# Performance work log

Measured on AMD Instinct MI355X. Metric: run time of the kernel, lower is better.

Reference implementation:

```python
import jax, jax.numpy as jnp
import numpy as np

TOPK = 10
NUM_CLASSES = 80
ALPHA = 0.5
BETA = 6.0
EPS = 1e-9


def setup_inputs() -> dict:
    key = jax.random.key(0)
    ks = jax.random.split(key, 7)
    bs, A, n, C = 16, 8400, 64, NUM_CLASSES
    pd_scores = jax.random.uniform(ks[0], (bs, A, C), jnp.float32)
    # valid xyxy boxes inside a 640x640 image
    pxy = jax.random.uniform(ks[1], (bs, A, 2), jnp.float32) * 576.0
    pwh = jax.random.uniform(ks[2], (bs, A, 2), jnp.float32) * 64.0 + 8.0
    pd_bboxes = jnp.concatenate([pxy, pxy + pwh], axis=-1)
    gxy = jax.random.uniform(ks[3], (bs, n, 2), jnp.float32) * 576.0
    gwh = jax.random.uniform(ks[4], (bs, n, 2), jnp.float32) * 64.0 + 8.0
    gt_bboxes = jnp.concatenate([gxy, gxy + gwh], axis=-1)
    anc_points = jax.random.uniform(ks[5], (A, 2), jnp.float32) * 640.0
    gt_labels = jax.random.randint(ks[6], (bs, n, 1), 0, C, dtype=jnp.int32)
    return {"pd_scores": pd_scores, "pd_bboxes": pd_bboxes,
            "anc_points": anc_points, "gt_labels": gt_labels,
            "gt_bboxes": gt_bboxes}


def _iou(gt_bboxes, pd_bboxes, eps=EPS):
    # gt_bboxes: (bs, n, 4), pd_bboxes: (bs, A, 4) -> (bs, n, A)
    b1 = gt_bboxes[:, :, None, :]
    b2 = pd_bboxes[:, None, :, :]
    lt = jnp.maximum(b1[..., :2], b2[..., :2])
    rb = jnp.minimum(b1[..., 2:], b2[..., 2:])
    overlap = jnp.clip(rb - lt, 0).prod(-1)
    area1 = jnp.clip(b1[..., 2:] - b1[..., :2], 0).prod(-1)
    area2 = jnp.clip(b2[..., 2:] - b2[..., :2], 0).prod(-1)
    return overlap / (area1 + area2 - overlap + eps)


def _assign(pd_scores, pd_bboxes, anc_points, gt_labels, gt_bboxes):
    bs, A, C = pd_scores.shape
    n = gt_bboxes.shape[1]
    dt = pd_scores.dtype
    labels = gt_labels[..., 0]                       # (bs, n)
    # ---- box metrics: gather class score per gt (bs, n, A) ----
    bi = jnp.arange(bs)[:, None]                     # (bs, 1)
    bbox_scores = pd_scores[bi, :, labels]           # (bs, n, A)
    overlaps = _iou(gt_bboxes, pd_bboxes)            # (bs, n, A)
    align_metric = bbox_scores ** ALPHA * overlaps ** BETA
    # ---- anchor-center-in-gt mask ----
    lt = gt_bboxes[..., None, :2]                    # (bs, n, 1, 2)
    rb = gt_bboxes[..., None, 2:]
    anc = anc_points[None, None]                     # (1, 1, A, 2)
    deltas_min = jnp.minimum((anc - lt).min(-1), (rb - anc).min(-1))
    mask_in_gts = (deltas_min > EPS).astype(dt)      # (bs, n, A)
    # ---- top-k candidates per gt (scatter-add instead of huge one-hot) ----
    metrics = align_metric * mask_in_gts
    topk_vals, topk_idxs = jax.lax.top_k(metrics, TOPK)
    valid = topk_vals.max(-1, keepdims=True) > EPS
    topk_idxs = jnp.where(valid, topk_idxs, 0)
    bi3 = jnp.arange(bs)[:, None, None]
    ni3 = jnp.arange(n)[None, :, None]
    cnt = jnp.zeros((bs, n, A), dt).at[bi3, ni3, topk_idxs].add(1.0)
    is_in_topk = jnp.where(cnt > 1, jnp.zeros((), dt), cnt)
    mask_pos = is_in_topk * mask_in_gts
    # ---- resolve anchors assigned to multiple gts via highest IoU ----
    fg_mask = mask_pos.sum(-2)                       # (bs, A)
    mask_multi = fg_mask[:, None, :] > 1             # (bs, 1->n, A)
    is_max = jax.nn.one_hot(overlaps.argmax(1), n, axis=1, dtype=dt)  # (bs, n, A)
    mask_pos = jnp.where(mask_multi, is_max, mask_pos)
    fg_mask = mask_pos.sum(-2)
    target_gt_idx = mask_pos.argmax(-2)              # (bs, A)
    # ---- gather targets ----
    flat_idx = target_gt_idx + jnp.arange(bs)[:, None] * n
    target_labels = jnp.maximum(labels.reshape(-1)[flat_idx], 0)
    target_bboxes = gt_bboxes.reshape(-1, 4)[flat_idx]
    target_scores = jax.nn.one_hot(target_labels, C, dtype=dt)
    target_scores = jnp.where(fg_mask[..., None] > 0, target_scores,
                              jnp.zeros((), dt))
    # ---- normalize scores by task-aligned metric ----
    align_metric = align_metric * mask_pos
    pos_align = align_metric.max(-1, keepdims=True)
    pos_over = (overlaps * mask_pos).max(-1, keepdims=True)
    norm = (align_metric * pos_over / (pos_align + EPS)).max(-2)[..., None]
    target_scores = target_scores * norm
    return target_labels, target_bboxes, target_scores, fg_mask > 0


def reference(pd_scores, pd_bboxes, anc_points, gt_labels, gt_bboxes):
    return _assign(pd_scores, pd_bboxes, anc_points, gt_labels, gt_bboxes)
```

## Files before the change

### kernel.cpp

```cpp
#include <hip/hip_runtime.h>

#define TOPK 10
#define EPSF 1e-9f

typedef unsigned long long u64;

__global__ __launch_bounds__(256) void k_init(uint4* __restrict__ p, int n16) {
    int i = blockIdx.x * 256 + threadIdx.x;
    if (i < n16) p[i] = make_uint4(0, 0, 0, 0);
}

__global__ __launch_bounds__(256) void k_row(
    const float* __restrict__ pd_scores, const float* __restrict__ pd_bboxes,
    const float* __restrict__ anc, const int* __restrict__ gt_labels,
    const float* __restrict__ gt_bboxes,
    float* __restrict__ overlaps, u64* __restrict__ mask64,
    int A, int n, int C)
{
    __shared__ float sv[256 * 11];
    __shared__ int   si[256 * 11];

    const int row = blockIdx.x;
    const int b   = row / n;
    const int j   = row - b * n;
    const int tid = threadIdx.x;

    const float4 g = *(const float4*)(gt_bboxes + (size_t)row * 4);
    const int    c = gt_labels[row];
    const float* ps = pd_scores + (size_t)b * A * C + c;
    const float4* pb = (const float4*)(pd_bboxes + (size_t)b * A * 4);
    const float2* an2 = (const float2*)anc;
    const size_t rowbase = (size_t)row * A;
    const float ga = fmaxf(g.z - g.x, 0.f) * fmaxf(g.w - g.y, 0.f);

    float tv[TOPK]; int ti[TOPK];
    #pragma unroll
    for (int k = 0; k < TOPK; ++k) { tv[k] = -1.f; ti[k] = 0x7fffffff; }

    for (int a = tid; a < A; a += 256) {
        float4 p = pb[a];
        float ow = fmaxf(fminf(g.z, p.z) - fmaxf(g.x, p.x), 0.f) *
                   fmaxf(fminf(g.w, p.w) - fmaxf(g.y, p.y), 0.f);
        float pa = fmaxf(p.z - p.x, 0.f) * fmaxf(p.w - p.y, 0.f);
        float iou = ow / (ga + pa - ow + EPSF);
        overlaps[rowbase + a] = iou;

        float2 ap = an2[a];
        float dmin = fminf(fminf(ap.x - g.x, ap.y - g.y),
                           fminf(g.z - ap.x, g.w - ap.y));
        float met = 0.f;
        if (dmin > EPSF) met = sqrtf(ps[(size_t)a * C]) * powf(iou, 6.0f);

        if (met > tv[TOPK-1] || (met == tv[TOPK-1] && a < ti[TOPK-1])) {
            tv[TOPK-1] = met; ti[TOPK-1] = a;
            #pragma unroll
            for (int k = TOPK-1; k > 0; --k) {
                if (tv[k] > tv[k-1] || (tv[k] == tv[k-1] && ti[k] < ti[k-1])) {
                    float fv = tv[k]; tv[k] = tv[k-1]; tv[k-1] = fv;
                    int   fi = ti[k]; ti[k] = ti[k-1]; ti[k-1] = fi;
                }
            }
        }
    }

    #pragma unroll
    for (int k = 0; k < TOPK; ++k) { sv[tid*11 + k] = tv[k]; si[tid*11 + k] = ti[k]; }

    for (int s = 128; s > 0; s >>= 1) {
        __syncthreads();
        if (tid < s) {
            const int bA = tid * 11, bB = (tid + s) * 11;
            int pa_ = 0, pb_ = 0;
            float ov[TOPK]; int oi[TOPK];
            #pragma unroll
            for (int k = 0; k < TOPK; ++k) {
                float va = sv[bA + pa_], vb = sv[bB + pb_];
                int   ja = si[bA + pa_], jb = si[bB + pb_];
                bool ta = (va > vb) || (va == vb && ja < jb);
                ov[k] = ta ? va : vb; oi[k] = ta ? ja : jb;
                pa_ += ta; pb_ += !ta;
            }
            #pragma unroll
            for (int k = 0; k < TOPK; ++k) { sv[bA + k] = ov[k]; si[bA + k] = oi[k]; }
        }
    }
    __syncthreads();

    if (sv[0] > EPSF && tid < TOPK) {
        int a = si[tid];
        float2 ap = an2[a];
        float dmin = fminf(fminf(ap.x - g.x, ap.y - g.y),
                           fminf(g.z - ap.x, g.w - ap.y));
        if (dmin > EPSF)
            atomicOr(&mask64[(size_t)b * A + a], 1ull << j);
    }
}

__global__ __launch_bounds__(256) void k_col(
    const float* __restrict__ pd_scores,
    const int* __restrict__ gt_labels, const float* __restrict__ gt_bboxes,
    const float* __restrict__ overlaps, u64* __restrict__ mask64,
    float* __restrict__ out_labels, float* __restrict__ out_bboxes,
    float* __restrict__ out_fg,
    float* __restrict__ pos_align, float* __restrict__ pos_over,
    int A, int n, int C)
{
    __shared__ float4 sg[64];
    __shared__ int    sl[64];
    const int b = blockIdx.y;
    const int a = blockIdx.x * 256 + threadIdx.x;
    if (threadIdx.x < n) {
        sg[threadIdx.x] = ((const float4*)gt_bboxes)[b * n + threadIdx.x];
        sl[threadIdx.x] = gt_labels[b * n + threadIdx.x];
    }
    __syncthreads();
    if (a >= A) return;

    const size_t midx = (size_t)b * A + a;
    u64 m = mask64[midx];
    int pc = __popcll(m);
    int jt = 0;
    if (pc > 1) {
        const float* col = overlaps + (size_t)b * n * A + a;
        float bv = col[0]; int bj = 0;
        for (int jj = 1; jj < n; ++jj) {
            float v = col[(size_t)jj * A];
            if (v > bv) { bv = v; bj = jj; }
        }
        jt = bj; mask64[midx] = 1ull << bj; pc = 1;
    } else if (pc == 1) {
        jt = __ffsll(m) - 1;
    }

    int lab = sl[jt];
    out_labels[midx] = (float)(lab < 0 ? 0 : lab);
    ((float4*)out_bboxes)[midx] = sg[jt];
    out_fg[midx] = pc ? 1.f : 0.f;

    if (pc) {
        int rowj = b * n + jt;
        float iou = overlaps[(size_t)rowj * A + a];
        float s = pd_scores[((size_t)b * A + a) * C + lab];
        float al = sqrtf(s) * powf(iou, 6.0f);
        atomicMax((int*)&pos_align[rowj], __float_as_int(al));
        atomicMax((int*)&pos_over[rowj],  __float_as_int(iou));
    }
}

__global__ __launch_bounds__(256) void k_norm(
    const float* __restrict__ pd_scores, const int* __restrict__ gt_labels,
    const float* __restrict__ overlaps, const u64* __restrict__ mask64,
    const float* __restrict__ pos_align, const float* __restrict__ pos_over,
    float* __restrict__ normv, int A, int n, int C, int total)
{
    int idx = blockIdx.x * 256 + threadIdx.x;
    if (idx >= total) return;
    int b = idx / A;
    int a = idx - b * A;
    u64 m = mask64[idx];
    float nm = 0.f;
    if (m) {
        int jj = __ffsll(m) - 1;
        int rowj = b * n + jj;
        float iou = overlaps[(size_t)rowj * A + a];
        float s = pd_scores[(size_t)idx * C + gt_labels[rowj]];
        float al = sqrtf(s) * powf(iou, 6.0f);
        nm = al * pos_over[rowj] / (pos_align[rowj] + EPSF);
    }
    normv[idx] = nm;
}

__global__ __launch_bounds__(256) void k_scores(
    const float* __restrict__ out_labels, const float* __restrict__ out_fg,
    const float* __restrict__ normv, float4* __restrict__ out_scores,
    int C4, int quads)
{
    int idx = blockIdx.x * 256 + threadIdx.x;
    if (idx >= quads) return;
    int ba = idx / C4;
    int q  = idx - ba * C4;
    float4 v = make_float4(0.f, 0.f, 0.f, 0.f);
    if (out_fg[ba] > 0.f) {
        int r = (int)out_labels[ba] - q * 4;
        float nv = normv[ba];
        v.x = (r == 0) ? nv : 0.f;
        v.y = (r == 1) ? nv : 0.f;
        v.z = (r == 2) ? nv : 0.f;
        v.w = (r == 3) ? nv : 0.f;
    }
    out_scores[idx] = v;
}

extern "C" void kernel_launch(void* const* d_in, const int* in_sizes, int n_in,
                              void* d_out, int out_size, void* d_ws, size_t ws_size,
                              hipStream_t stream)
{
    const float* pd_scores = (const float*)d_in[0];
    const float* pd_bboxes = (const float*)d_in[1];
    const float* anc       = (const float*)d_in[2];
    const int*   gt_labels = (const int*)d_in[3];
    const float* gt_bboxes = (const float*)d_in[4];

    const int C  = 80;
    const int A  = in_sizes[2] / 2;
    const int bs = in_sizes[0] / (A * C);
    const int n  = in_sizes[3] / bs;
    const int R  = bs * n;
    const int BA = bs * A;

    size_t off = 0;
    u64*   mask64    = (u64*)((char*)d_ws + off);   off += (size_t)BA * 8;
    float* pos_align = (float*)((char*)d_ws + off); off += (size_t)R * 4;
    float* pos_over  = (float*)((char*)d_ws + off); off += (size_t)R * 4;
    size_t zero_bytes = off;
    float* overlaps  = (float*)((char*)d_ws + off); off += (size_t)R * A * 4;
    float* normv     = (float*)((char*)d_ws + off); off += (size_t)BA * 4;

    float* out_labels = (float*)d_out;
    float* out_bboxes = out_labels + (size_t)BA;
    float* out_scores = out_bboxes + (size_t)BA * 4;
    float* out_fg     = out_scores + (size_t)BA * C;

    int n16 = (int)(zero_bytes / 16);
    k_init<<<(n16 + 255) / 256, 256, 0, stream>>>((uint4*)d_ws, n16);

    k_row<<<R, 256, 0, stream>>>(
        pd_scores, pd_bboxes, anc, gt_labels, gt_bboxes, overlaps, mask64, A, n, C);

    k_col<<<dim3((A + 255) / 256, bs), 256, 0, stream>>>(
        pd_scores, gt_labels, gt_bboxes, overlaps, mask64,
        out_labels, out_bboxes, out_fg, pos_align, pos_over, A, n, C);

    k_norm<<<(BA + 255) / 256, 256, 0, stream>>>(
        pd_scores, gt_labels, overlaps, mask64, pos_align, pos_over,
        normv, A, n, C, BA);

    int quads = BA * (C / 4);
    k_scores<<<(quads + 255) / 256, 256, 0, stream>>>(
        out_labels, out_fg, normv, (float4*)out_scores, C / 4, quads);
}
```

Measured before the change: 173.5 us.

## Split per-GT top-k scan across anchor chunks and merge partial lists

The per-row top-k kernel is split into four anchor chunks per GT row, so the grid grows from R to 4R blocks, each writing a partial top-10 list. A new merge kernel combines the four sorted lists per row and sets the mask bits. Value and index are also packed into one 64-bit key, so comparisons and shared-memory traffic use a single u64. This gives more parallelism over the 1024 rows at the cost of an extra launch and the same tree reduction running four times per row.

```diff
diff --git a/kernel.cpp b/kernel.cpp
--- a/kernel.cpp
+++ b/kernel.cpp
@@ -2,28 +2,31 @@
 
 #define TOPK 10
 #define EPSF 1e-9f
+#define CHUNKS 4
 
 typedef unsigned long long u64;
+typedef unsigned int u32;
 
 __global__ __launch_bounds__(256) void k_init(uint4* __restrict__ p, int n16) {
     int i = blockIdx.x * 256 + threadIdx.x;
     if (i < n16) p[i] = make_uint4(0, 0, 0, 0);
 }
 
-__global__ __launch_bounds__(256) void k_row(
+__global__ __launch_bounds__(256) void k_chunk(
     const float* __restrict__ pd_scores, const float* __restrict__ pd_bboxes,
     const float* __restrict__ anc, const int* __restrict__ gt_labels,
     const float* __restrict__ gt_bboxes,
-    float* __restrict__ overlaps, u64* __restrict__ mask64,
+    float* __restrict__ overlaps, u64* __restrict__ part,
     int A, int n, int C)
 {
-    __shared__ float sv[256 * 11];
-    __shared__ int   si[256 * 11];
-
-    const int row = blockIdx.x;
+    __shared__ u64 sk[256 * 11];
+
+    const int row = blockIdx.y;
     const int b   = row / n;
-    const int j   = row - b * n;
     const int tid = threadIdx.x;
+    const int CS  = (A + CHUNKS - 1) / CHUNKS;
+    const int a0  = blockIdx.x * CS;
+    const int a1  = min(A, a0 + CS);
 
     const float4 g = *(const float4*)(gt_bboxes + (size_t)row * 4);
     const int    c = gt_labels[row];
@@ -33,11 +36,11 @@
     const size_t rowbase = (size_t)row * A;
     const float ga = fmaxf(g.z - g.x, 0.f) * fmaxf(g.w - g.y, 0.f);
 
-    float tv[TOPK]; int ti[TOPK];
+    u64 tk[TOPK];
     #pragma unroll
-    for (int k = 0; k < TOPK; ++k) { tv[k] = -1.f; ti[k] = 0x7fffffff; }
-
-    for (int a = tid; a < A; a += 256) {
+    for (int k = 0; k < TOPK; ++k) tk[k] = 0;
+
+    for (int a = a0 + tid; a < a1; a += 256) {
         float4 p = pb[a];
         float ow = fmaxf(fminf(g.z, p.z) - fmaxf(g.x, p.x), 0.f) *
                    fmaxf(fminf(g.w, p.w) - fmaxf(g.y, p.y), 0.f);
@@ -51,43 +54,72 @@
         float met = 0.f;
         if (dmin > EPSF) met = sqrtf(ps[(size_t)a * C]) * powf(iou, 6.0f);
 
-        if (met > tv[TOPK-1] || (met == tv[TOPK-1] && a < ti[TOPK-1])) {
-            tv[TOPK-1] = met; ti[TOPK-1] = a;
+        u64 key = ((u64)__float_as_uint(met) << 32) | (u32)(0x7fffffff - a);
+        if (key > tk[TOPK-1]) {
+            tk[TOPK-1] = key;
             #pragma unroll
-            for (int k = TOPK-1; k > 0; --k) {
-                if (tv[k] > tv[k-1] || (tv[k] == tv[k-1] && ti[k] < ti[k-1])) {
-                    float fv = tv[k]; tv[k] = tv[k-1]; tv[k-1] = fv;
-                    int   fi = ti[k]; ti[k] = ti[k-1]; ti[k-1] = fi;
-                }
-            }
+            for (int k = TOPK-1; k > 0; --k)
+                if (tk[k] > tk[k-1]) { u64 t = tk[k]; tk[k] = tk[k-1]; tk[k-1] = t; }
         }
     }
 
     #pragma unroll
-    for (int k = 0; k < TOPK; ++k) { sv[tid*11 + k] = tv[k]; si[tid*11 + k] = ti[k]; }
+    for (int k = 0; k < TOPK; ++k) sk[tid * 11 + k] = tk[k];
 
     for (int s = 128; s > 0; s >>= 1) {
         __syncthreads();
         if (tid < s) {
             const int bA = tid * 11, bB = (tid + s) * 11;
             int pa_ = 0, pb_ = 0;
-            float ov[TOPK]; int oi[TOPK];
+            u64 out[TOPK];
             #pragma unroll
             for (int k = 0; k < TOPK; ++k) {
-                float va = sv[bA + pa_], vb = sv[bB + pb_];
-                int   ja = si[bA + pa_], jb = si[bB + pb_];
-                bool ta = (va > vb) || (va == vb && ja < jb);
-                ov[k] = ta ? va : vb; oi[k] = ta ? ja : jb;
+                u64 va = sk[bA + pa_], vb = sk[bB + pb_];
+                bool ta = va > vb;
+                out[k] = ta ? va : vb;
                 pa_ += ta; pb_ += !ta;
             }
             #pragma unroll
-            for (int k = 0; k < TOPK; ++k) { sv[bA + k] = ov[k]; si[bA + k] = oi[k]; }
+            for (int k = 0; k < TOPK; ++k) sk[bA + k] = out[k];
         }
     }
     __syncthreads();
 
-    if (sv[0] > EPSF && tid < TOPK) {
-        int a = si[tid];
+    if (tid < TOPK)
+        part[((size_t)row * CHUNKS + blockIdx.x) * TOPK + tid] = sk[tid];
+}
+
+__global__ __launch_bounds__(256) void k_merge(
+    const float* __restrict__ anc, const float* __restrict__ gt_bboxes,
+    const u64* __restrict__ part, u64* __restrict__ mask64,
+    int A, int n, int R)
+{
+    int row = blockIdx.x * 256 + threadIdx.x;
+    if (row >= R) return;
+    int b = row / n;
+    int j = row - b * n;
+    const u64* l = part + (size_t)row * CHUNKS * TOPK;
+    const float4 g = *(const float4*)(gt_bboxes + (size_t)row * 4);
+    const float2* an2 = (const float2*)anc;
+
+    int p0 = 0, p1 = 0, p2 = 0, p3 = 0;
+    for (int k = 0; k < TOPK; ++k) {
+        u64 v0 = (p0 < TOPK) ? l[p0]            : 0;
+        u64 v1 = (p1 < TOPK) ? l[TOPK + p1]     : 0;
+        u64 v2 = (p2 < TOPK) ? l[2 * TOPK + p2] : 0;
+        u64 v3 = (p3 < TOPK) ? l[3 * TOPK + p3] : 0;
+        u64 bv = v0; int best = 0;
+        if (v1 > bv) { bv = v1; best = 1; }
+        if (v2 > bv) { bv = v2; best = 2; }
+        if (v3 > bv) { bv = v3; best = 3; }
+        p0 += (best == 0); p1 += (best == 1);
+        p2 += (best == 2); p3 += (best == 3);
+
+        if (k == 0) {
+            float m0 = __uint_as_float((u32)(bv >> 32));
+            if (!(m0 > EPSF)) break;
+        }
+        int a = 0x7fffffff - (int)(u32)(bv & 0xffffffffu);
         float2 ap = an2[a];
         float dmin = fminf(fminf(ap.x - g.x, ap.y - g.y),
                            fminf(g.z - ap.x, g.w - ap.y));
@@ -215,6 +247,7 @@
     size_t zero_bytes = off;
     float* overlaps  = (float*)((char*)d_ws + off); off += (size_t)R * A * 4;
     float* normv     = (float*)((char*)d_ws + off); off += (size_t)BA * 4;
+    u64*   part      = (u64*)((char*)d_ws + off);   off += (size_t)R * CHUNKS * TOPK * 8;
 
     float* out_labels = (float*)d_out;
     float* out_bboxes = out_labels + (size_t)BA;
@@ -224,8 +257,11 @@
     int n16 = (int)(zero_bytes / 16);
     k_init<<<(n16 + 255) / 256, 256, 0, stream>>>((uint4*)d_ws, n16);
 
-    k_row<<<R, 256, 0, stream>>>(
-        pd_scores, pd_bboxes, anc, gt_labels, gt_bboxes, overlaps, mask64, A, n, C);
+    k_chunk<<<dim3(CHUNKS, R), 256, 0, stream>>>(
+        pd_scores, pd_bboxes, anc, gt_labels, gt_bboxes, overlaps, part, A, n, C);
+
+    k_merge<<<(R + 255) / 256, 256, 0, stream>>>(
+        anc, gt_bboxes, part, mask64, A, n, R);
 
     k_col<<<dim3((A + 255) / 256, bs), 256, 0, stream>>>(
         pd_scores, gt_labels, gt_bboxes, overlaps, mask64,
```

Measured after the change: 172.5 us. Within noise of the previous version (-0.5%).
